# Optimization experiments

Measured on AMD Instinct MI355X. Metric: run time of the kernel, lower is better.

## Reference

```python
import jax, jax.numpy as jnp
import numpy as np


def setup_inputs() -> dict:
    key = jax.random.key(0)
    ks = jax.random.split(key, 8)
    B, T, I, H, D, V = 8, 256, 256, 512, 32, 256
    x = jax.random.normal(ks[0], (B, T, I), jnp.float32)
    lengths = jax.random.randint(ks[1], (B,), 1, T + 1, dtype=jnp.int32)
    aff_w = jax.random.normal(ks[2], (I, H), jnp.float32) / np.sqrt(I)
    aff_b = jnp.zeros((H,), jnp.float32)
    xav = np.sqrt(6.0 / (H + H))
    lateral = jax.random.uniform(ks[3], (H, H), jnp.float32, -xav, xav)
    eff_w = jax.random.normal(ks[4], (H, V), jnp.float32) / np.sqrt(H)
    eff_b = jnp.zeros((V,), jnp.float32)
    tau = D * jax.random.uniform(ks[5], (H, H), jnp.float32) + 1.0
    return dict(x=x, lengths=lengths, aff_w=aff_w, aff_b=aff_b, lateral=lateral,
                eff_w=eff_w, eff_b=eff_b, tau=tau, N=64, max_delay=32,
                max_think_steps=16)


def _credit_matrix(tau, max_delay, key, dtype):
    # training-mode straight-through Gumbel selection over delay axis
    tau_c = jnp.clip(tau, 1.0, max_delay)[None]                 # (1,H,H)
    d_ax = jnp.arange(max_delay + 1, dtype=dtype)[:, None, None]
    raw = (1.0 + jnp.abs(d_ax - tau_c)) ** (-0.5)
    logits = jnp.log(raw + 1e-8)
    u = jax.random.uniform(key, logits.shape, dtype)
    g = -jnp.log(-jnp.log(u + 1e-8) + 1e-8)
    pert = logits + g
    soft = jax.nn.softmax(pert, axis=0)
    hard = jax.nn.one_hot(jnp.argmax(pert, axis=0), max_delay + 1, axis=0, dtype=dtype)
    return soft + jax.lax.stop_gradient(hard - soft)               # (D+1,H,H)


def reference(x, lengths, aff_w, aff_b, lateral, eff_w, eff_b, tau,
              N, max_delay, max_think_steps):
    B, T, I = x.shape
    H = lateral.shape[0]
    V = eff_w.shape[1]
    D = max_delay
    think_end = V - 1
    key = jax.random.key(42)

    credit = _credit_matrix(tau, D, jax.random.fold_in(key, 0), x.dtype)
    W = credit[1:] * lateral[None]                                 # (D,H,H)
    W_rev = W[::-1]

    def step_fast(x_t, history, ptr):
        W_al = jnp.roll(W_rev, ptr, axis=0)                       # (D,H,H)
        h_del = jnp.einsum('dhi,dbi->bh', W_al, history)          # (B,H)
        h_new = jnp.tanh(x_t @ aff_w + aff_b + h_del)
        mask = (jnp.arange(D) == ptr)[:, None, None]
        history = jnp.where(mask, h_new[None], history)
        return history, (ptr + 1) % D, h_del @ eff_w + eff_b

    # ---------------- encoder pass over T -------------------------------
    def enc_body(carry, inp):
        history, ptr, sh, sp = carry
        x_t, t = inp
        history, ptr, _ = step_fast(x_t, history, ptr)
        last = (t == lengths - 1)                                  # (B,)
        sh = jnp.where(last[None, :, None], history, sh)
        sp = jnp.where(last, ptr, sp)
        return (history, ptr, sh, sp), None

    h0 = jnp.zeros((D, B, H), x.dtype)
    carry0 = (h0, jnp.int32(0), h0, jnp.zeros((B,), jnp.int32))
    (_, _, saved_h, saved_p), _ = jax.lax.scan(
        enc_body, carry0, (x.transpose(1, 0, 2), jnp.arange(T)))

    # align per-sample circular buffers so ptr = 0
    history = jax.vmap(lambda h, p: jnp.roll(h, -p, axis=0),
                       in_axes=(1, 0), out_axes=1)(saved_h, saved_p)
    ptr = jnp.int32(0)
    curr = x[jnp.arange(B), lengths - 1, :]
    is_done = jnp.zeros((B,), bool)
    tst = jnp.zeros((B,), jnp.int32)
    last_valid = curr

    # ---------------- thinking phase (frozen once all done) -------------
    def think_body(carry, s):
        history, ptr, curr, is_done, tst, last_valid = carry
        active = ~jnp.all(is_done)
        nh, nptr, y = step_fast(curr, history, ptr)
        g = jax.random.gumbel(jax.random.fold_in(key, 1000 + s), y.shape, y.dtype)
        sampled = jnp.argmax(y + g, axis=-1)
        adj = y  # input_size == vocab_size so _adjust_dim is identity
        just = (sampled == think_end) & ~is_done
        nlv = jnp.where(is_done[:, None], last_valid, adj)
        ntst = tst + (~is_done).astype(jnp.int32)
        ndone = is_done | just
        ncurr = adj * (~ndone)[:, None].astype(adj.dtype)
        new = (nh, nptr, ncurr, ndone, ntst, nlv)
        old = (history, ptr, curr, is_done, tst, last_valid)
        return jax.tree.map(lambda a, b: jnp.where(active, a, b), new, old), None

    (history, ptr, curr, is_done, tst, last_valid), _ = jax.lax.scan(
        think_body, (history, ptr, curr, is_done, tst, last_valid),
        jnp.arange(max_think_steps))
    curr = last_valid

    # ---------------- decoding phase over N -----------------------------
    def dec_body(carry, j):
        history, ptr, curr = carry
        history, ptr, y = step_fast(curr, history, ptr)
        g = jax.random.gumbel(jax.random.fold_in(key, 2000 + j), y.shape, y.dtype)
        soft = jax.nn.softmax(y + g, axis=-1)
        hard = jax.nn.one_hot(jnp.argmax(soft, axis=-1), V, dtype=y.dtype)
        one_hot_out = soft + jax.lax.stop_gradient(hard - soft)
        return (history, ptr, one_hot_out), y

    _, ys = jax.lax.scan(dec_body, (history, ptr, curr), jnp.arange(N))
    outputs = ys.transpose(1, 0, 2)[:, :, :-1]                     # (B,N,V-1)
    return outputs, tst
```

## Files before the change

kernel.cpp:

```cpp
#include <hip/hip_runtime.h>
#include <hip/hip_bf16.h>
#include <stdint.h>
#include <stddef.h>

#define NB 8
#define TT 256
#define IDIM 256
#define HH 512
#define VV 256
#define DD 32
#define NDEC 64
#define NTHINK 16
#define HCB 8
#define HSL 64
#define NTHR 1024

#define HEX_OFF 0u
#define YEX_OFF 65536u
#define FEX_OFF 327680u
#define DLY_OFF 328704u
#define EXZ_BYTES 328704u

__device__ __forceinline__ void pubf(uint64_t* p, float v, uint32_t stamp){
  const uint64_t pk = ((uint64_t)stamp << 32) | (uint64_t)__float_as_uint(v);
  __hip_atomic_store(p, pk, __ATOMIC_RELAXED, __HIP_MEMORY_SCOPE_AGENT);
}
__device__ __forceinline__ float waitf(uint64_t* p, uint32_t stamp){
  uint64_t pk;
  do { pk = __hip_atomic_load(p, __ATOMIC_RELAXED, __HIP_MEMORY_SCOPE_AGENT); }
  while ((uint32_t)(pk >> 32) != stamp);
  return __uint_as_float((uint32_t)pk);
}

__device__ __forceinline__ void tfr(uint32_t &x0, uint32_t &x1, int r){
  x0 += x1; x1 = (x1 << r) | (x1 >> (32 - r)); x1 ^= x0;
}
__device__ __forceinline__ void threefry(uint32_t k0, uint32_t k1,
                                         uint32_t c0, uint32_t c1,
                                         uint32_t &o0, uint32_t &o1){
  const uint32_t k2 = k0 ^ k1 ^ 0x1BD11BDAu;
  uint32_t x0 = c0 + k0, x1 = c1 + k1;
  tfr(x0,x1,13); tfr(x0,x1,15); tfr(x0,x1,26); tfr(x0,x1,6);
  x0 += k1; x1 += k2 + 1u;
  tfr(x0,x1,17); tfr(x0,x1,29); tfr(x0,x1,16); tfr(x0,x1,24);
  x0 += k2; x1 += k0 + 2u;
  tfr(x0,x1,13); tfr(x0,x1,15); tfr(x0,x1,26); tfr(x0,x1,6);
  x0 += k0; x1 += k1 + 3u;
  tfr(x0,x1,17); tfr(x0,x1,29); tfr(x0,x1,16); tfr(x0,x1,24);
  x0 += k1; x1 += k2 + 4u;
  tfr(x0,x1,13); tfr(x0,x1,15); tfr(x0,x1,26); tfr(x0,x1,6);
  x0 += k2; x1 += k0 + 5u;
  o0 = x0; o1 = x1;
}
__device__ __forceinline__ uint32_t pbits(uint32_t k0, uint32_t k1, uint32_t i){
  uint32_t o0, o1; threefry(k0, k1, 0u, i, o0, o1);
  return o0 ^ o1;
}
__device__ __forceinline__ float bits_to_unit(uint32_t bits){
  return __uint_as_float((bits >> 9) | 0x3F800000u) - 1.0f;
}

__global__ __launch_bounds__(256) void delays_kernel(
    const float* __restrict__ tau, unsigned char* __restrict__ dl)
{
  const int e = blockIdx.x * 256 + threadIdx.x;
  if (e >= HH*HH) return;
  uint32_t kc0, kc1; threefry(0u, 42u, 0u, 0u, kc0, kc1);
  const float tcf = fminf(fmaxf(tau[e], 1.0f), 32.0f);
  const double tc = (double)tcf;
  double best = -1.0e300; int am = 0;
  for (int d = 0; d <= DD; ++d){
    const uint32_t f = (uint32_t)d * (uint32_t)(HH*HH) + (uint32_t)e;
    const double u = (double)bits_to_unit(pbits(kc0, kc1, f));
    const double raw = 1.0 / sqrt(1.0 + fabs((double)d - tc));
    const double pert = log(raw + 1e-8) - log(-log(u + 1e-8) + 1e-8);
    if (pert > best){ best = pert; am = d; }
  }
  dl[e] = (unsigned char)am;
}

__global__ __launch_bounds__(NTHR) void seq_kernel(
    const float* __restrict__ x, const int* __restrict__ lengths,
    const float* __restrict__ aff_w, const float* __restrict__ aff_b,
    const float* __restrict__ eff_w, const float* __restrict__ eff_b,
    const float* __restrict__ lateral, const unsigned char* __restrict__ dl,
    uint64_t* __restrict__ hex_, uint64_t* __restrict__ yex,
    uint64_t* __restrict__ fex, float* __restrict__ out)
{
  extern __shared__ double smd[];
  double* curr  = smd;
  double* lastv = curr + 256;
  double* ypq   = lastv + 256;
  double* hdels = ypq + 1024;
  double* redv  = hdels + 64;
  float*  hist  = (float*)(redv + 4);
  float*  effs  = hist + 32*513;
  float*  effbs = effs + 64*256;
  int*    redi  = (int*)(effbs + 256);
  int*    misc  = redi + 4;

  const int tid = threadIdx.x;
  const int b   = blockIdx.x & 7;
  const int hc  = blockIdx.x >> 3;
  const int hl  = tid >> 4;
  const int p   = tid & 15;
  const int h   = hc * HSL + hl;

  float w[32]; uint32_t dpk[8]; float aw[16];
  #pragma unroll
  for (int k = 0; k < 32; ++k){
    const int idx = h*HH + p + 16*k;
    const int d = (int)dl[idx];
    w[k] = (d >= 1) ? lateral[idx] : 0.0f;
    dpk[k >> 2] = (k & 3) ? (dpk[k >> 2] | ((uint32_t)d << ((k & 3)*8)))
                          : (uint32_t)d;
  }
  #pragma unroll
  for (int m = 0; m < 16; ++m) aw[m] = aff_w[(p + 16*m)*HH + h];
  const double ab = (double)aff_b[h];

  for (int q = tid; q < 32*513; q += NTHR) hist[q] = 0.0f;
  for (int q = tid; q < HSL*VV; q += NTHR) effs[q] = eff_w[hc*HSL*VV + q];
  if (tid < VV) effbs[tid] = eff_b[tid];
  __syncthreads();

  const int L = lengths[b];
  int t = 0;
  uint32_t stamp = 0;

  auto gather = [&](double &hd, double &af){
    const int tm = t & 31;
    double a0 = 0.0, a1 = 0.0;
    #pragma unroll
    for (int k = 0; k < 32; ++k){
      const int d = (int)((dpk[k >> 2] >> ((k & 3)*8)) & 0xFFu);
      const int row = (tm - d) & 31;
      a0 += (double)w[k] * (double)hist[row*513 + p + 16*k];
    }
    #pragma unroll
    for (int m = 0; m < 16; ++m) a1 += (double)aw[m] * curr[p + 16*m];
    #pragma unroll
    for (int m = 1; m < 16; m <<= 1){
      a0 += __shfl_xor(a0, m, 64);
      a1 += __shfl_xor(a1, m, 64);
    }
    hd = a0; af = a1;
  };

  auto ypartial = [&](){
    const int q = tid >> 8, v = tid & 255;
    double acc = 0.0;
    #pragma unroll
    for (int m = 0; m < 16; ++m)
      acc += hdels[q*16 + m] * (double)effs[(q*16 + m)*VV + v];
    ypq[q*256 + v] = acc;
  };

  auto argmax256 = [&](double pr){
    if (tid < VV){
      double bv = pr; int bi = tid;
      #pragma unroll
      for (int m = 1; m < 64; m <<= 1){
        const double ov = __shfl_xor(bv, m, 64);
        const int    oi = __shfl_xor(bi, m, 64);
        if (ov > bv || (ov == bv && oi < bi)){ bv = ov; bi = oi; }
      }
      if ((tid & 63) == 0){ redv[tid >> 6] = bv; redi[tid >> 6] = bi; }
    }
    __syncthreads();
    if (tid == 0){
      double bv = redv[0]; int bi = redi[0];
      #pragma unroll
      for (int q2 = 1; q2 < 4; ++q2)
        if (redv[q2] > bv || (redv[q2] == bv && redi[q2] < bi)){ bv = redv[q2]; bi = redi[q2]; }
      misc[0] = bi;
    }
    __syncthreads();
  };

  auto gumbel_t = [&](uint32_t base, int sv) -> double {
    uint32_t k0, k1; threefry(0u, 42u, 0u, base + (uint32_t)sv, k0, k1);
    const uint32_t f = (uint32_t)(b*VV + tid);
    float u = bits_to_unit(pbits(k0, k1, f));
    if (u < 1.1754944e-38f) u = 1.1754944e-38f;
    return log(-log((double)u));
  };

  for (; t < L; ){
    if (tid < IDIM) curr[tid] = (double)x[(b*TT + t)*IDIM + tid];
    __syncthreads();
    double hd, af; gather(hd, af);
    const double hn = tanh(hd + af + ab);
    const uint32_t stp = ++stamp;
    const int par = (int)(stp & 1u);
    uint64_t* slab = hex_ + (par*NB + b)*HH;
    if (p == 0) pubf(slab + h, (float)hn, stp);
    if (tid < HH) hist[(t & 31)*513 + tid] = waitf(slab + tid, stp);
    ++t;
  }

  if (tid < IDIM){
    const double xv = (double)x[(b*TT + (L-1))*IDIM + tid];
    curr[tid] = xv; lastv[tid] = xv;
  }
  __syncthreads();

  bool done = false; int tst = 0;
  for (int s = 0; s < NTHINK; ++s){
    double hd, af; gather(hd, af);
    const double hn = tanh(hd + af + ab);
    const uint32_t stp = ++stamp;
    const int par = (int)(stp & 1u);
    uint64_t* slab = hex_ + (par*NB + b)*HH;
    uint64_t* yslab = yex + ((par*NB + b)*HCB)*VV;
    if (p == 0){ pubf(slab + h, (float)hn, stp); hdels[hl] = hd; }
    if (hc == 0 && tid == 0)
      __hip_atomic_store(fex + s*NB + b, (uint64_t)(done ? 2u : 1u),
                         __ATOMIC_RELAXED, __HIP_MEMORY_SCOPE_AGENT);
    __syncthreads();
    ypartial();
    __syncthreads();
    if (tid < VV)
      pubf(yslab + hc*VV + tid,
           (float)(ypq[tid] + ypq[256 + tid] + ypq[512 + tid] + ypq[768 + tid]), stp);
    if (tid < NB){
      uint64_t v;
      do { v = __hip_atomic_load(fex + s*NB + tid, __ATOMIC_RELAXED,
                                 __HIP_MEMORY_SCOPE_AGENT); } while (v == 0ull);
      misc[2 + tid] = (v == 2ull);
    }
    __syncthreads();
    if (tid == 0){
      int ad = 1;
      #pragma unroll
      for (int bb = 0; bb < NB; ++bb) ad &= misc[2 + bb];
      misc[1] = ad;
    }
    __syncthreads();
    if (misc[1]) break;
    if (tid < HH) hist[(t & 31)*513 + tid] = waitf(slab + tid, stp);
    double yv = 0.0, pr = 0.0;
    if (tid < VV){
      double acc = (double)effbs[tid];
      float part[8]; uint32_t need = 0xFFu;
      while (need){
        #pragma unroll
        for (int c = 0; c < HCB; ++c) if (need & (1u << c)){
          const uint64_t pk = __hip_atomic_load(yslab + c*VV + tid,
                              __ATOMIC_RELAXED, __HIP_MEMORY_SCOPE_AGENT);
          if ((uint32_t)(pk >> 32) == stp){
            part[c] = __uint_as_float((uint32_t)pk); need &= ~(1u << c);
          }
        }
      }
      #pragma unroll
      for (int c = 0; c < HCB; ++c) acc += (double)part[c];
      yv = acc;
      pr = yv - gumbel_t(1000u, s);
    }
    argmax256(pr);
    const int sampled = misc[0];
    const bool just = (sampled == VV - 1) && !done;
    if (!done){
      ++tst;
      if (tid < VV) lastv[tid] = yv;
    }
    const bool nd = done || just;
    if (tid < VV) curr[tid] = nd ? 0.0 : yv;
    done = nd;
    ++t;
    __syncthreads();
  }

  if (tid < VV) curr[tid] = lastv[tid];
  __syncthreads();
  for (int dj = 0; dj < NDEC; ++dj){
    double hd, af; gather(hd, af);
    const double hn = tanh(hd + af + ab);
    const uint32_t stp = ++stamp;
    const int par = (int)(stp & 1u);
    uint64_t* slab = hex_ + (par*NB + b)*HH;
    uint64_t* yslab = yex + ((par*NB + b)*HCB)*VV;
    if (p == 0){ pubf(slab + h, (float)hn, stp); hdels[hl] = hd; }
    __syncthreads();
    ypartial();
    __syncthreads();
    if (tid < VV)
      pubf(yslab + hc*VV + tid,
           (float)(ypq[tid] + ypq[256 + tid] + ypq[512 + tid] + ypq[768 + tid]), stp);
    if (tid < HH) hist[(t & 31)*513 + tid] = waitf(slab + tid, stp);
    double yv = 0.0, pr = 0.0;
    if (tid < VV){
      double acc = (double)effbs[tid];
      float part[8]; uint32_t need = 0xFFu;
      while (need){
        #pragma unroll
        for (int c = 0; c < HCB; ++c) if (need & (1u << c)){
          const uint64_t pk = __hip_atomic_load(yslab + c*VV + tid,
                              __ATOMIC_RELAXED, __HIP_MEMORY_SCOPE_AGENT);
          if ((uint32_t)(pk >> 32) == stp){
            part[c] = __uint_as_float((uint32_t)pk); need &= ~(1u << c);
          }
        }
      }
      #pragma unroll
      for (int c = 0; c < HCB; ++c) acc += (double)part[c];
      yv = acc;
      if (hc == 0 && tid < VV - 1)
        out[(b*NDEC + dj)*(VV - 1) + tid] = (float)yv;
      pr = yv - gumbel_t(2000u, dj);
    }
    argmax256(pr);
    const int sampled = misc[0];
    if (tid < VV) curr[tid] = (tid == sampled) ? 1.0 : 0.0;
    ++t;
    __syncthreads();
  }
  if (hc == 0 && tid == 0) out[NB*NDEC*(VV-1) + b] = (float)tst;
}

extern "C" void kernel_launch(void* const* d_in, const int* in_sizes, int n_in,
                              void* d_out, int out_size, void* d_ws, size_t ws_size,
                              hipStream_t stream)
{
  (void)in_sizes; (void)n_in; (void)out_size; (void)ws_size;
  const float* x     = (const float*)d_in[0];
  const int*   len   = (const int*)  d_in[1];
  const float* affw  = (const float*)d_in[2];
  const float* affb  = (const float*)d_in[3];
  const float* later = (const float*)d_in[4];
  const float* effw  = (const float*)d_in[5];
  const float* effb  = (const float*)d_in[6];
  const float* tau   = (const float*)d_in[7];

  char* ws = (char*)d_ws;
  uint64_t* hex_     = (uint64_t*)(ws + HEX_OFF);
  uint64_t* yex      = (uint64_t*)(ws + YEX_OFF);
  uint64_t* fex      = (uint64_t*)(ws + FEX_OFF);
  unsigned char* dl  = (unsigned char*)(ws + DLY_OFF);

  hipMemsetAsync(ws, 0, EXZ_BYTES, stream);
  delays_kernel<<<dim3((HH*HH)/256), dim3(256), 0, stream>>>(tau, dl);

  const int smem = (256 + 256 + 1024 + 64 + 4) * 8
                 + (32*513 + 64*256 + 256) * 4 + 20 * 4;
  hipFuncSetAttribute((const void*)seq_kernel,
                      hipFuncAttributeMaxDynamicSharedMemorySize, smem);
  seq_kernel<<<dim3(64), dim3(NTHR), smem, stream>>>(
      x, len, affw, affb, effw, effb, later, dl, hex_, yex, fex,
      (float*)d_out);
}
```

Before: 3.602 ms.

## Split delayed-history gather to overlap cross-block exchange wait with old-delay work

The lateral weights are split into delay-1 terms and older-delay terms. The older-delay contribution and the input projection are now computed before waiting for the previous step's hidden-state exchange from other blocks, so that inter-block latency is hidden behind useful work. The x input is read directly from global memory rather than staged through shared memory. The think-phase done-flag polling is folded into the same barrier, which removes two syncs. The logit partial gather is now spread across all threads into shared memory instead of each thread spin-polling all 8 chunks. The cost is more registers (two weight arrays) and a more complex stamp and parity schedule.

```diff
diff --git a/kernel.cpp b/kernel.cpp
--- a/kernel.cpp
+++ b/kernel.cpp
@@ -96,7 +96,8 @@
   float*  hist  = (float*)(redv + 4);
   float*  effs  = hist + 32*513;
   float*  effbs = effs + 64*256;
-  int*    redi  = (int*)(effbs + 256);
+  float*  ypl   = effbs + 256;
+  int*    redi  = (int*)(ypl + 2048);
   int*    misc  = redi + 4;
 
   const int tid = threadIdx.x;
@@ -106,12 +107,14 @@
   const int p   = tid & 15;
   const int h   = hc * HSL + hl;
 
-  float w[32]; uint32_t dpk[8]; float aw[16];
+  float w_old[32], w1[32]; uint32_t dpk[8]; float aw[16];
   #pragma unroll
   for (int k = 0; k < 32; ++k){
     const int idx = h*HH + p + 16*k;
     const int d = (int)dl[idx];
-    w[k] = (d >= 1) ? lateral[idx] : 0.0f;
+    const float wv = (d >= 1) ? lateral[idx] : 0.0f;
+    w1[k]    = (d == 1) ? wv : 0.0f;
+    w_old[k] = (d == 1) ? 0.0f : wv;
     dpk[k >> 2] = (k & 3) ? (dpk[k >> 2] | ((uint32_t)d << ((k & 3)*8)))
                           : (uint32_t)d;
   }
@@ -125,28 +128,29 @@
   __syncthreads();
 
   const int L = lengths[b];
-  int t = 0;
-  uint32_t stamp = 0;
-
-  auto gather = [&](double &hd, double &af){
-    const int tm = t & 31;
-    double a0 = 0.0, a1 = 0.0;
+  uint32_t st = 0;
+
+  auto aold = [&](double &a0){
+    const int tm = (int)(st & 31u);
+    a0 = 0.0;
     #pragma unroll
     for (int k = 0; k < 32; ++k){
       const int d = (int)((dpk[k >> 2] >> ((k & 3)*8)) & 0xFFu);
       const int row = (tm - d) & 31;
-      a0 += (double)w[k] * (double)hist[row*513 + p + 16*k];
-    }
-    #pragma unroll
-    for (int m = 0; m < 16; ++m) a1 += (double)aw[m] * curr[p + 16*m];
+      a0 += (double)w_old[k] * (double)hist[row*513 + p + 16*k];
+    }
+  };
+  auto anew_reduce = [&](double &a0, double &a1){
+    const int rn = (int)((st + 31u) & 31u);
+    #pragma unroll
+    for (int k = 0; k < 32; ++k)
+      a0 += (double)w1[k] * (double)hist[rn*513 + p + 16*k];
     #pragma unroll
     for (int m = 1; m < 16; m <<= 1){
       a0 += __shfl_xor(a0, m, 64);
       a1 += __shfl_xor(a1, m, 64);
     }
-    hd = a0; af = a1;
-  };
-
+  };
   auto ypartial = [&](){
     const int q = tid >> 8, v = tid & 255;
     double acc = 0.0;
@@ -155,7 +159,6 @@
       acc += hdels[q*16 + m] * (double)effs[(q*16 + m)*VV + v];
     ypq[q*256 + v] = acc;
   };
-
   auto argmax256 = [&](double pr){
     if (tid < VV){
       double bv = pr; int bi = tid;
@@ -177,7 +180,6 @@
     }
     __syncthreads();
   };
-
   auto gumbel_t = [&](uint32_t base, int sv) -> double {
     uint32_t k0, k1; threefry(0u, 42u, 0u, base + (uint32_t)sv, k0, k1);
     const uint32_t f = (uint32_t)(b*VV + tid);
@@ -186,75 +188,74 @@
     return log(-log((double)u));
   };
 
-  for (; t < L; ){
-    if (tid < IDIM) curr[tid] = (double)x[(b*TT + t)*IDIM + tid];
-    __syncthreads();
-    double hd, af; gather(hd, af);
-    const double hn = tanh(hd + af + ab);
-    const uint32_t stp = ++stamp;
-    const int par = (int)(stp & 1u);
-    uint64_t* slab = hex_ + (par*NB + b)*HH;
-    if (p == 0) pubf(slab + h, (float)hn, stp);
-    if (tid < HH) hist[(t & 31)*513 + tid] = waitf(slab + tid, stp);
-    ++t;
+  for (; st < (uint32_t)L; ){
+    double a0, a1 = 0.0;
+    aold(a0);
+    {
+      const float* xr = x + ((size_t)b*TT + st)*IDIM + p;
+      #pragma unroll
+      for (int m = 0; m < 16; ++m) a1 += (double)aw[m] * (double)xr[16*m];
+    }
+    uint64_t* slabR = hex_ + ((st & 1u)*NB + b)*HH;
+    if (tid < HH) hist[(int)((st + 31u) & 31u)*513 + tid] = waitf(slabR + tid, st);
+    __syncthreads();
+    anew_reduce(a0, a1);
+    const double hn = tanh(a0 + a1 + ab);
+    if (p == 0) pubf(hex_ + (((st + 1u) & 1u)*NB + b)*HH + h, (float)hn, st + 1u);
+    ++st;
   }
 
   if (tid < IDIM){
-    const double xv = (double)x[(b*TT + (L-1))*IDIM + tid];
+    const double xv = (double)x[((size_t)b*TT + (L-1))*IDIM + tid];
     curr[tid] = xv; lastv[tid] = xv;
   }
   __syncthreads();
 
   bool done = false; int tst = 0;
   for (int s = 0; s < NTHINK; ++s){
-    double hd, af; gather(hd, af);
-    const double hn = tanh(hd + af + ab);
-    const uint32_t stp = ++stamp;
-    const int par = (int)(stp & 1u);
-    uint64_t* slab = hex_ + (par*NB + b)*HH;
-    uint64_t* yslab = yex + ((par*NB + b)*HCB)*VV;
-    if (p == 0){ pubf(slab + h, (float)hn, stp); hdels[hl] = hd; }
+    double a0, a1 = 0.0;
+    aold(a0);
+    #pragma unroll
+    for (int m = 0; m < 16; ++m) a1 += (double)aw[m] * curr[p + 16*m];
     if (hc == 0 && tid == 0)
       __hip_atomic_store(fex + s*NB + b, (uint64_t)(done ? 2u : 1u),
                          __ATOMIC_RELAXED, __HIP_MEMORY_SCOPE_AGENT);
+    uint64_t* slabR = hex_ + ((st & 1u)*NB + b)*HH;
+    if (tid < HH){
+      hist[(int)((st + 31u) & 31u)*513 + tid] = waitf(slabR + tid, st);
+    } else if (tid < HH + NB){
+      uint64_t v;
+      do { v = __hip_atomic_load(fex + s*NB + (tid - HH), __ATOMIC_RELAXED,
+                                 __HIP_MEMORY_SCOPE_AGENT); } while (v == 0ull);
+      misc[2 + (tid - HH)] = (v == 2ull);
+    }
+    __syncthreads();
+    {
+      int ad = 1;
+      #pragma unroll
+      for (int bb = 0; bb < NB; ++bb) ad &= misc[2 + bb];
+      if (ad) break;
+    }
+    anew_reduce(a0, a1);
+    const double hn = tanh(a0 + a1 + ab);
+    const uint32_t sw = st + 1u;
+    const int parW = (int)(sw & 1u);
+    if (p == 0){ pubf(hex_ + (parW*NB + b)*HH + h, (float)hn, sw); hdels[hl] = a0; }
     __syncthreads();
     ypartial();
     __syncthreads();
+    uint64_t* ybase = yex + ((size_t)(parW*NB + b)*HCB)*VV;
     if (tid < VV)
-      pubf(yslab + hc*VV + tid,
-           (float)(ypq[tid] + ypq[256 + tid] + ypq[512 + tid] + ypq[768 + tid]), stp);
-    if (tid < NB){
-      uint64_t v;
-      do { v = __hip_atomic_load(fex + s*NB + tid, __ATOMIC_RELAXED,
-                                 __HIP_MEMORY_SCOPE_AGENT); } while (v == 0ull);
-      misc[2 + tid] = (v == 2ull);
-    }
-    __syncthreads();
-    if (tid == 0){
-      int ad = 1;
-      #pragma unroll
-      for (int bb = 0; bb < NB; ++bb) ad &= misc[2 + bb];
-      misc[1] = ad;
-    }
-    __syncthreads();
-    if (misc[1]) break;
-    if (tid < HH) hist[(t & 31)*513 + tid] = waitf(slab + tid, stp);
+      pubf(ybase + hc*VV + tid,
+           (float)(ypq[tid] + ypq[256 + tid] + ypq[512 + tid] + ypq[768 + tid]), sw);
+    ypl[tid]        = waitf(ybase + tid, sw);
+    ypl[tid + 1024] = waitf(ybase + tid + 1024, sw);
+    __syncthreads();
     double yv = 0.0, pr = 0.0;
     if (tid < VV){
       double acc = (double)effbs[tid];
-      float part[8]; uint32_t need = 0xFFu;
-      while (need){
-        #pragma unroll
-        for (int c = 0; c < HCB; ++c) if (need & (1u << c)){
-          const uint64_t pk = __hip_atomic_load(yslab + c*VV + tid,
-                              __ATOMIC_RELAXED, __HIP_MEMORY_SCOPE_AGENT);
-          if ((uint32_t)(pk >> 32) == stp){
-            part[c] = __uint_as_float((uint32_t)pk); need &= ~(1u << c);
-          }
-        }
-      }
-      #pragma unroll
-      for (int c = 0; c < HCB; ++c) acc += (double)part[c];
+      #pragma unroll
+      for (int c = 0; c < HCB; ++c) acc += (double)ypl[c*VV + tid];
       yv = acc;
       pr = yv - gumbel_t(1000u, s);
     }
@@ -268,52 +269,49 @@
     const bool nd = done || just;
     if (tid < VV) curr[tid] = nd ? 0.0 : yv;
     done = nd;
-    ++t;
+    ++st;
     __syncthreads();
   }
 
   if (tid < VV) curr[tid] = lastv[tid];
   __syncthreads();
   for (int dj = 0; dj < NDEC; ++dj){
-    double hd, af; gather(hd, af);
-    const double hn = tanh(hd + af + ab);
-    const uint32_t stp = ++stamp;
-    const int par = (int)(stp & 1u);
-    uint64_t* slab = hex_ + (par*NB + b)*HH;
-    uint64_t* yslab = yex + ((par*NB + b)*HCB)*VV;
-    if (p == 0){ pubf(slab + h, (float)hn, stp); hdels[hl] = hd; }
+    double a0, a1 = 0.0;
+    aold(a0);
+    #pragma unroll
+    for (int m = 0; m < 16; ++m) a1 += (double)aw[m] * curr[p + 16*m];
+    uint64_t* slabR = hex_ + ((st & 1u)*NB + b)*HH;
+    if (tid < HH) hist[(int)((st + 31u) & 31u)*513 + tid] = waitf(slabR + tid, st);
+    __syncthreads();
+    anew_reduce(a0, a1);
+    const double hn = tanh(a0 + a1 + ab);
+    const uint32_t sw = st + 1u;
+    const int parW = (int)(sw & 1u);
+    if (p == 0){ pubf(hex_ + (parW*NB + b)*HH + h, (float)hn, sw); hdels[hl] = a0; }
     __syncthreads();
     ypartial();
     __syncthreads();
+    uint64_t* ybase = yex + ((size_t)(parW*NB + b)*HCB)*VV;
     if (tid < VV)
-      pubf(yslab + hc*VV + tid,
-           (float)(ypq[tid] + ypq[256 + tid] + ypq[512 + tid] + ypq[768 + tid]), stp);
-    if (tid < HH) hist[(t & 31)*513 + tid] = waitf(slab + tid, stp);
+      pubf(ybase + hc*VV + tid,
+           (float)(ypq[tid] + ypq[256 + tid] + ypq[512 + tid] + ypq[768 + tid]), sw);
+    ypl[tid]        = waitf(ybase + tid, sw);
+    ypl[tid + 1024] = waitf(ybase + tid + 1024, sw);
+    __syncthreads();
     double yv = 0.0, pr = 0.0;
     if (tid < VV){
       double acc = (double)effbs[tid];
-      float part[8]; uint32_t need = 0xFFu;
-      while (need){
-        #pragma unroll
-        for (int c = 0; c < HCB; ++c) if (need & (1u << c)){
-          const uint64_t pk = __hip_atomic_load(yslab + c*VV + tid,
-                              __ATOMIC_RELAXED, __HIP_MEMORY_SCOPE_AGENT);
-          if ((uint32_t)(pk >> 32) == stp){
-            part[c] = __uint_as_float((uint32_t)pk); need &= ~(1u << c);
-          }
-        }
-      }
-      #pragma unroll
-      for (int c = 0; c < HCB; ++c) acc += (double)part[c];
+      #pragma unroll
+      for (int c = 0; c < HCB; ++c) acc += (double)ypl[c*VV + tid];
       yv = acc;
       if (hc == 0 && tid < VV - 1)
-        out[(b*NDEC + dj)*(VV - 1) + tid] = (float)yv;
+        out[((size_t)b*NDEC + dj)*(VV - 1) + tid] = (float)yv;
       pr = yv - gumbel_t(2000u, dj);
     }
     argmax256(pr);
     const int sampled = misc[0];
     if (tid < VV) curr[tid] = (tid == sampled) ? 1.0 : 0.0;
-    ++t;
+    ++st;
     __syncthreads();
   }
   if (hc == 0 && tid == 0) out[NB*NDEC*(VV-1) + b] = (float)tst;
@@ -343,7 +341,7 @@
   delays_kernel<<<dim3((HH*HH)/256), dim3(256), 0, stream>>>(tau, dl);
 
   const int smem = (256 + 256 + 1024 + 64 + 4) * 8
-                 + (32*513 + 64*256 + 256) * 4 + 20 * 4;
+                 + (32*513 + 64*256 + 256 + 2048) * 4 + 20 * 4;
   hipFuncSetAttribute((const void*)seq_kernel,
                       hipFuncAttributeMaxDynamicSharedMemorySize, smem);
   seq_kernel<<<dim3(64), dim3(NTHR), smem, stream>>>(
```

Result: slower. 8.077 ms (+124.2%).
